# Kernel tuning notes

Hardware: AMD Instinct MI355X
Metric: run time of the kernel (lower is better)

The kernel has to match this reference:

```python
import jax, jax.numpy as jnp
import numpy as np

B, S, D, H, MLP = 8, 1024, 768, 12, 3072
HD = D // H
EPS = 1e-5


def setup_inputs() -> dict:
    key = jax.random.key(0)
    ks = jax.random.split(key, 5)
    sd = lambda fan_in: 1.0 / np.sqrt(fan_in)
    return {
        "x": jax.random.normal(ks[0], (B, S, D), jnp.float32),
        "w_qkv": jax.random.normal(ks[1], (D, 3 * D), jnp.float32) * sd(D),
        "w_out": jax.random.normal(ks[2], (D, D), jnp.float32) * sd(D),
        "b_out": jnp.zeros((D,), jnp.float32),
        "w1": jax.random.normal(ks[3], (D, MLP), jnp.float32) * sd(D),
        "b1": jnp.zeros((MLP,), jnp.float32),
        "w2": jax.random.normal(ks[4], (MLP, D), jnp.float32) * sd(MLP),
        "b2": jnp.zeros((D,), jnp.float32),
    }


def _instance_norm(x):
    # torch InstanceNorm2d on a 3D [B,S,D] tensor treats it as unbatched (C,H,W):
    # normalize over (S, D) per batch element, biased var, eps=1e-5, no affine.
    mu = jnp.mean(x, axis=(1, 2), keepdims=True)
    var = jnp.mean(jnp.square(x - mu), axis=(1, 2), keepdims=True)
    return (x - mu) * jax.lax.rsqrt(var + EPS)


def reference(x, w_qkv, w_out, b_out, w1, b1, w2, b2):
    scale = HD ** -0.5
    # --- self-attention branch ---
    h = _instance_norm(x)
    qkv = (h @ w_qkv).reshape(B, S, 3, H, HD)          # (qkv, heads, head_dim) split
    qkv = qkv.transpose(2, 0, 3, 1, 4)                  # [3, B, H, S, HD]
    q, k, v = qkv[0], qkv[1], qkv[2]
    att = jax.nn.softmax(jnp.einsum('bhxd,bhyd->bhxy', q, k) * scale, axis=-1)
    o = jnp.einsum('bhxy,bhyd->bhxd', att, v)           # [B, H, S, HD]
    o = o.transpose(0, 2, 1, 3).reshape(B, S, D)        # b h l d -> b l (h d)
    x = x + (o @ w_out + b_out)
    # --- MLP branch (exact erf GELU, as nn.GELU default) ---
    h2 = _instance_norm(x)
    m = jax.nn.gelu(h2 @ w1 + b1, approximate=False) @ w2 + b2
    return x + m
```

## Files before the change

kernel.cpp:

```cpp
#include <hip/hip_runtime.h>
#include <hip/hip_bf16.h>

typedef __hip_bfloat16 bf16;
typedef __attribute__((ext_vector_type(8))) short short8;
typedef __attribute__((ext_vector_type(4))) float f32x4;

#define B_   8
#define S_   1024
#define D_   768
#define H_   12
#define HD_  64
#define MLP_ 3072
#define SD_  (S_ * D_)

#define QSCALE 0.18033688011112042f

__device__ __forceinline__ float b2f(short h) {
  union { unsigned u; float f; } w;
  w.u = ((unsigned)(unsigned short)h) << 16;
  return w.f;
}

__device__ __forceinline__ float fast_exp2(float x) {
  float r;
  asm("v_exp_f32 %0, %1" : "=v"(r) : "v"(x));
  return r;
}

__device__ __forceinline__ bf16 fastbf(float f) {
  union { float f; unsigned u; } w; w.f = f;
  unsigned r = (w.u + 0x7FFF + ((w.u >> 16) & 1)) >> 16;
  union { unsigned short s; bf16 b; } o; o.s = (unsigned short)r;
  return o.b;
}

__device__ __forceinline__ void gl2lds16(const bf16* g, bf16* l) {
  __builtin_amdgcn_global_load_lds(
      (const __attribute__((address_space(1))) unsigned*)(const void*)g,
      (__attribute__((address_space(3))) unsigned*)(void*)l, 16, 0, 0);
}

__global__ __launch_bounds__(256) void transpose_all(
    const float* __restrict__ w_qkv, const float* __restrict__ w_out,
    const float* __restrict__ w1, const float* __restrict__ w2,
    bf16* __restrict__ t_qkv, bf16* __restrict__ t_out,
    bf16* __restrict__ t1, bf16* __restrict__ t2,
    float* __restrict__ zstats) {
  const int t = blockIdx.x;
  if (t == 0 && threadIdx.x < 32) zstats[threadIdx.x] = 0.f;
  const float* in; bf16* out; int R, C, idx;
  if (t < 1728)      { in = w_qkv; out = t_qkv; R = 768;  C = 2304; idx = t; }
  else if (t < 2304) { in = w_out; out = t_out; R = 768;  C = 768;  idx = t - 1728; }
  else if (t < 4608) { in = w1;    out = t1;    R = 768;  C = 3072; idx = t - 2304; }
  else               { in = w2;    out = t2;    R = 3072; C = 768;  idx = t - 4608; }
  const int nbx = C >> 5;
  const int bx = (idx % nbx) * 32, by = (idx / nbx) * 32;
  __shared__ float tt[32][33];
  const int tx = threadIdx.x & 31, ty = threadIdx.x >> 5;
#pragma unroll
  for (int rr = 0; rr < 32; rr += 8)
    tt[ty + rr][tx] = in[(long)(by + ty + rr) * C + bx + tx];
  __syncthreads();
#pragma unroll
  for (int rr = 0; rr < 32; rr += 8)
    out[(long)(bx + ty + rr) * R + by + tx] = __float2bfloat16(tt[tx][ty + rr]);
}

__global__ __launch_bounds__(256) void stats_partial(const float* __restrict__ x,
                                                     float* __restrict__ red_x,
                                                     const bf16* __restrict__ wt1,
                                                     const bf16* __restrict__ wt_qkv,
                                                     float* __restrict__ cs1,
                                                     float* __restrict__ csq,
                                                     bf16* __restrict__ xb) {
  if (blockIdx.x >= 768) {
    const bf16* wsrc; float* cdst; int bi;
    if (blockIdx.x < 816) { wsrc = wt1;    cdst = cs1; bi = blockIdx.x - 768; }
    else                  { wsrc = wt_qkv; cdst = csq; bi = blockIdx.x - 816; }
    const int row = bi * 64 + (threadIdx.x >> 2);
    const int part = threadIdx.x & 3;
    const bf16* wr = wsrc + (long)row * 768 + part * 192;
    float s = 0.f;
#pragma unroll
    for (int u = 0; u < 24; ++u) {
      short8 v = *(const short8*)(wr + u * 8);
#pragma unroll
      for (int e = 0; e < 8; ++e) s += b2f(v[e]);
    }
    s += __shfl_xor(s, 1, 64);
    s += __shfl_xor(s, 2, 64);
    if (part == 0) cdst[row] = s;
    return;
  }
  const long off = (long)blockIdx.x * 8192;
  float s = 0.f, s2 = 0.f;
#pragma unroll
  for (int it = 0; it < 4; ++it) {
    const long i = off + ((long)threadIdx.x + it * 256) * 8;
    float4 v0 = *(const float4*)(x + i);
    float4 v1 = *(const float4*)(x + i + 4);
    s += v0.x + v0.y + v0.z + v0.w + v1.x + v1.y + v1.z + v1.w;
    s2 += v0.x * v0.x + v0.y * v0.y + v0.z * v0.z + v0.w * v0.w +
          v1.x * v1.x + v1.y * v1.y + v1.z * v1.z + v1.w * v1.w;
    __align__(16) bf16 tmp[8];
    tmp[0] = __float2bfloat16(v0.x); tmp[1] = __float2bfloat16(v0.y);
    tmp[2] = __float2bfloat16(v0.z); tmp[3] = __float2bfloat16(v0.w);
    tmp[4] = __float2bfloat16(v1.x); tmp[5] = __float2bfloat16(v1.y);
    tmp[6] = __float2bfloat16(v1.z); tmp[7] = __float2bfloat16(v1.w);
    *(short8*)(xb + i) = *(const short8*)tmp;
  }
#pragma unroll
  for (int o = 1; o < 64; o <<= 1) { s += __shfl_xor(s, o, 64); s2 += __shfl_xor(s2, o, 64); }
  __shared__ float sh[8];
  const int wave = threadIdx.x >> 6, lane = threadIdx.x & 63;
  if (lane == 0) { sh[wave * 2] = s; sh[wave * 2 + 1] = s2; }
  __syncthreads();
  if (threadIdx.x == 0) {
    const int bb = blockIdx.x / 96;
    atomicAdd(&red_x[bb * 2],     sh[0] + sh[2] + sh[4] + sh[6]);
    atomicAdd(&red_x[bb * 2 + 1], sh[1] + sh[3] + sh[5] + sh[7]);
  }
}

template <int EPI, bool STATS>
__global__ __launch_bounds__(256) void gemm_k(
    const bf16* __restrict__ A, const bf16* __restrict__ Bt,
    int M, int N, int K,
    const float* __restrict__ biasf, const float* __restrict__ resf,
    const float* __restrict__ cs, const float* __restrict__ stat_in,
    float* __restrict__ outf,
    bf16* __restrict__ outb0, bf16* __restrict__ outb1, bf16* __restrict__ outb2,
    float* __restrict__ statp) {
  __shared__ __align__(16) bf16 As[128 * 64];
  __shared__ __align__(16) bf16 Bs[128 * 64];
  __shared__ float sred[8];
  const int tid = threadIdx.x;
  const int bm = blockIdx.x * 128, bn = blockIdx.y * 128;
  const int wave = tid >> 6, lane = tid & 63;
  const int quad = lane >> 4, l16 = lane & 15;
  const int wm = (wave >> 1) * 64, wn = (wave & 1) * 64;
  const int swz = l16 & 7;

  f32x4 acc[4][4];
#pragma unroll
  for (int i = 0; i < 4; ++i)
#pragma unroll
    for (int j = 0; j < 4; ++j) acc[i][j] = (f32x4){0.f, 0.f, 0.f, 0.f};

  const int srow = tid >> 3;
  const int sgc = (tid & 7) ^ (srow & 7);
  const bf16* Ab = A + (long)(bm + srow) * K + sgc * 8;
  const bf16* Bb = Bt + (long)(bn + srow) * K + sgc * 8;

  auto stage = [&](int k0) {
#pragma unroll
    for (int s = 0; s < 4; ++s)
      gl2lds16(Ab + (long)(s * 32) * K + k0, &As[0] + s * 2048 + tid * 8);
#pragma unroll
    for (int s = 0; s < 4; ++s)
      gl2lds16(Bb + (long)(s * 32) * K + k0, &Bs[0] + s * 2048 + tid * 8);
  };

  stage(0);
  const int nk = K >> 6;
  for (int kt = 0; kt < nk; ++kt) {
    __syncthreads();
    short8 a[2][4], b[2][4];
#pragma unroll
    for (int kk = 0; kk < 2; ++kk) {
      const int co = ((kk * 4 + quad) ^ swz) * 8;
#pragma unroll
      for (int i = 0; i < 4; ++i)
        a[kk][i] = *(const short8*)(&As[0] + (wm + i * 16 + l16) * 64 + co);
#pragma unroll
      for (int j = 0; j < 4; ++j)
        b[kk][j] = *(const short8*)(&Bs[0] + (wn + j * 16 + l16) * 64 + co);
    }
    __syncthreads();
    if (kt + 1 < nk) stage((kt + 1) * 64);
#pragma unroll
    for (int kk = 0; kk < 2; ++kk)
#pragma unroll
      for (int i = 0; i < 4; ++i)
#pragma unroll
        for (int j = 0; j < 4; ++j)
          acc[i][j] = __builtin_amdgcn_mfma_f32_16x16x32_bf16(a[kk][i], b[kk][j], acc[i][j], 0, 0, 0);
  }

  const int m0 = bm + wm + quad * 4;
  const int n0 = bn + wn + l16;
  const int batch = bm >> 10;
  float mu = 0.f, rs = 0.f;
  if (EPI == 0 || EPI == 2) {
    const float s1 = stat_in[batch * 2], s2v = stat_in[batch * 2 + 1];
    mu = s1 * (1.0f / SD_);
    rs = rsqrtf(s2v * (1.0f / SD_) - mu * mu + 1e-5f);
  }
  float ts = 0.f, ts2 = 0.f;
#pragma unroll
  for (int i = 0; i < 4; ++i) {
#pragma unroll
    for (int j = 0; j < 4; ++j) {
      const int n = n0 + j * 16;
#pragma unroll
      for (int r = 0; r < 4; ++r) {
        const int m = m0 + i * 16 + r;
        float v = acc[i][j][r];
        if (EPI == 0) {
          v = rs * (v - mu * cs[n]);
          const int t = n / D_;
          const int rr2 = n - t * D_;
          const int hh = rr2 >> 6, dd = rr2 & 63;
          const int bb = m >> 10, ss = m & 1023;
          const long hoff = (long)(bb * H_ + hh);
          if (t == 0)      outb0[(hoff * S_ + ss) * HD_ + dd] = __float2bfloat16(v * QSCALE);
          else if (t == 1) outb1[(hoff * S_ + ss) * HD_ + dd] = __float2bfloat16(v);
          else             outb2[(hoff * HD_ + dd) * S_ + ss] = __float2bfloat16(v);
        } else if (EPI == 1) {
          v += biasf[n] + resf[(long)m * N + n];
          outf[(long)m * N + n] = v;
          outb0[(long)m * N + n] = __float2bfloat16(v);
          if (STATS) { ts += v; ts2 += v * v; }
        } else if (EPI == 2) {
          v = rs * (v - mu * cs[n]) + biasf[n];
          float u = v * v;
          float y = v * (1.0f + 0.044715f * u) * 0.7978845608028654f;
          float z = fast_exp2(y * -2.885390081777927f);
          v = v * __builtin_amdgcn_rcpf(1.0f + z);
          outb0[(long)m * N + n] = __float2bfloat16(v);
        } else {
          v += biasf[n] + resf[(long)m * N + n];
          outf[(long)m * N + n] = v;
        }
      }
    }
  }
  if (STATS) {
#pragma unroll
    for (int o = 1; o < 64; o <<= 1) { ts += __shfl_xor(ts, o, 64); ts2 += __shfl_xor(ts2, o, 64); }
    if (lane == 0) { sred[wave * 2] = ts; sred[wave * 2 + 1] = ts2; }
    __syncthreads();
    if (tid == 0) {
      atomicAdd(&statp[batch * 2], sred[0] + sred[2] + sred[4] + sred[6]);
      atomicAdd(&statp[batch * 2 + 1], sred[1] + sred[3] + sred[5] + sred[7]);
    }
  }
}

__global__ __launch_bounds__(512) void attn64(const bf16* __restrict__ q,
                                              const bf16* __restrict__ k,
                                              const bf16* __restrict__ vt,
                                              bf16* __restrict__ o) {
  __shared__ __align__(16) bf16 Ks[2][64 * 64];
  __shared__ __align__(16) bf16 Vs[2][64 * 64];
  const int bh = blockIdx.x, qt = blockIdx.y;
  const int tid = threadIdx.x, wave = tid >> 6, lane = tid & 63;
  const int quad = lane >> 4, l16 = lane & 15;
  const int sw = (l16 & 7) ^ ((l16 >> 3) & 1);
  const long base = (long)bh * (S_ * HD_);
  const bf16* kg = k + base;
  const bf16* vg = vt + base;

  const int srow = tid >> 3;
  const int scg = (tid & 7) ^ (srow & 7) ^ ((srow >> 3) & 1);

  short8 aq[2];
#pragma unroll
  for (int kk = 0; kk < 2; ++kk)
    aq[kk] = *(const short8*)(q + base + (long)(qt * 128 + wave * 16 + l16) * HD_ +
                              kk * 32 + quad * 8);

  gl2lds16(kg + (long)srow * HD_ + scg * 8, &Ks[0][0] + tid * 8);
  gl2lds16(vg + (long)srow * S_ + scg * 8, &Vs[0][0] + tid * 8);

  const bf16* kp = kg + (long)(64 + srow) * HD_ + scg * 8;
  const bf16* vp = vg + (long)srow * S_ + 64 + scg * 8;

  f32x4 oacc[4];
#pragma unroll
  for (int j = 0; j < 4; ++j) oacc[j] = (f32x4){0.f, 0.f, 0.f, 0.f};
  float lp = 0.f;

  const int vh = (quad & 1) * 4;

#define ATTN_STEP(CUR, DOPREF)                                                 \
  {                                                                            \
    __syncthreads();                                                           \
    if (DOPREF) {               \
      gl2lds16(kp, &Ks[(CUR) ^ 1][0] + tid * 8);                               \
      gl2lds16(vp, &Vs[(CUR) ^ 1][0] + tid * 8);                               \
      kp += 64 * HD_;                                                          \
      vp += 64;                                                                \
    }                                                                          \
    f32x4 s[4];                                                                \
    _Pragma("unroll")                                                          \
    for (int i = 0; i < 4; ++i) s[i] = (f32x4){0.f, 0.f, 0.f, 0.f};            \
    _Pragma("unroll")                                                          \
    for (int kk = 0; kk < 2; ++kk) {                                           \
      _Pragma("unroll")                                                        \
      for (int i = 0; i < 4; ++i) {                                            \
        short8 ak = *(const short8*)(&Ks[CUR][0] + (i * 16 + l16) * 64 +       \
                                     (((kk * 4 + quad) ^ sw) * 8));            \
        s[i] = __builtin_amdgcn_mfma_f32_16x16x32_bf16(ak, aq[kk], s[i], 0, 0, 0); \
      }                                                                        \
    }                                                                          \
    float pe[4][4];                                                            \
    _Pragma("unroll")                                                          \
    for (int i = 0; i < 4; ++i) {                                              \
      _Pragma("unroll")                                                        \
      for (int r = 0; r < 4; ++r) { pe[i][r] = fast_exp2(s[i][r]); lp += pe[i][r]; } \
    }                                                                          \
    union { short8 v; bf16 b[8]; } af[2];                                      \
    _Pragma("unroll")                                                          \
    for (int r = 0; r < 4; ++r) {                                              \
      af[0].b[r]     = fastbf(pe[0][r]);                                       \
      af[0].b[4 + r] = fastbf(pe[1][r]);                                       \
      af[1].b[r]     = fastbf(pe[2][r]);                                       \
      af[1].b[4 + r] = fastbf(pe[3][r]);                                       \
    }                                                                          \
    _Pragma("unroll")                                                          \
    for (int kk = 0; kk < 2; ++kk) {                                           \
      const int g0 = ((4 * kk + (quad >> 1)) ^ sw) * 8 + vh;                   \
      const int g1 = ((4 * kk + 2 + (quad >> 1)) ^ sw) * 8 + vh;               \
      _Pragma("unroll")                                                        \
      for (int dj = 0; dj < 4; ++dj) {                                         \
        const bf16* vrow = &Vs[CUR][0] + (dj * 16 + l16) * 64;                 \
        union { short8 v; uint2 u[2]; } bv;                                    \
        bv.u[0] = *(const uint2*)(vrow + g0);                                  \
        bv.u[1] = *(const uint2*)(vrow + g1);                                  \
        oacc[dj] = __builtin_amdgcn_mfma_f32_16x16x32_bf16(af[kk].v, bv.v, oacc[dj], 0, 0, 0); \
      }                                                                        \
    }                                                                          \
  }

  for (int c = 0; c < 16; c += 2) {
    ATTN_STEP(0, true)
    ATTN_STEP(1, (c < 14))
  }
#undef ATTN_STEP

  float lt = lp;
  lt += __shfl_xor(lt, 16, 64);
  lt += __shfl_xor(lt, 32, 64);

  const int b = bh / H_, hh = bh - b * H_;
#pragma unroll
  for (int r = 0; r < 4; ++r) {
    const float inv = 1.0f / __shfl(lt, quad * 4 + r, 64);
    const int sg = qt * 128 + wave * 16 + quad * 4 + r;
    const long rowoff = ((long)b * S_ + sg) * D_ + hh * HD_;
#pragma unroll
    for (int dj = 0; dj < 4; ++dj)
      o[rowoff + dj * 16 + l16] = __float2bfloat16(oacc[dj][r] * inv);
  }
}

extern "C" void kernel_launch(void* const* d_in, const int* in_sizes, int n_in,
                              void* d_out, int out_size, void* d_ws, size_t ws_size,
                              hipStream_t stream) {
  const float* x     = (const float*)d_in[0];
  const float* w_qkv = (const float*)d_in[1];
  const float* w_out = (const float*)d_in[2];
  const float* b_out = (const float*)d_in[3];
  const float* w1    = (const float*)d_in[4];
  const float* b1    = (const float*)d_in[5];
  const float* w2    = (const float*)d_in[6];
  const float* b2    = (const float*)d_in[7];
  float* out = (float*)d_out;

  bf16* wt_qkv = (bf16*)d_ws;
  bf16* wt_out = wt_qkv + 2304 * 768;
  bf16* wt1    = wt_out + 768 * 768;
  bf16* wt2    = wt1 + 3072 * 768;
  bf16* qb     = wt2 + 768 * 3072;
  bf16* kb     = qb + 6291456;
  bf16* vtb    = kb + 6291456;
  bf16* ob     = vtb + 6291456;
  float* x1f   = (float*)(ob + 6291456);
  bf16* hb     = (bf16*)(x1f + 6291456);
  float* redp  = (float*)(hb + 6291456);
  float* red_x = redp + 1536;
  float* red2  = red_x + 16;
  float* cs1   = red2 + 16;
  float* csq   = cs1 + 3072;
  bf16* gb     = qb;
  bf16* xb     = hb;
  bf16* x1b    = hb;

  transpose_all<<<6912, 256, 0, stream>>>(w_qkv, w_out, w1, w2,
                                          wt_qkv, wt_out, wt1, wt2, red_x);

  stats_partial<<<768 + 48 + 36, 256, 0, stream>>>(x, red_x, wt1, wt_qkv,
                                                   cs1, csq, xb);

  gemm_k<0, false><<<dim3(64, 18), 256, 0, stream>>>(
      xb, wt_qkv, 8192, 2304, 768, nullptr, nullptr, csq, red_x,
      nullptr, qb, kb, vtb, nullptr);
  attn64<<<dim3(B_ * H_, 8), 512, 0, stream>>>(qb, kb, vtb, ob);

  gemm_k<1, true><<<dim3(64, 6), 256, 0, stream>>>(
      ob, wt_out, 8192, 768, 768, b_out, x, nullptr, nullptr,
      x1f, x1b, nullptr, nullptr, red2);

  gemm_k<2, false><<<dim3(64, 24), 256, 0, stream>>>(
      x1b, wt1, 8192, 3072, 768, b1, nullptr, cs1, red2,
      nullptr, gb, nullptr, nullptr, nullptr);

  gemm_k<3, false><<<dim3(64, 6), 256, 0, stream>>>(
      gb, wt2, 8192, 768, 3072, b2, x1f, nullptr, nullptr,
      out, nullptr, nullptr, nullptr, nullptr);
}
```

Baseline: 341.7 us.

## Merge weight transpose and input stats into one kernel; add attention MFMA priority hints

Fuses the weight transpose/convert kernel with the input-statistics and column-sum work into a single launch. Column sums are now computed directly from the fp32 weights with bf16 rounding, removing the dependency on the transposed output. Per-block partial sums replace atomics, and the QKV GEMM reduces the 96 partials per batch in its epilogue. The attention loop also wraps its MFMA sections in s_setprio hints. The trade-offs are strided, poorly coalesced column-sum loads in a few long-running blocks and a redundant 96-element reduction in every GEMM block.

Result: slower. 352.5 us (+3.2%).

```diff
diff --git a/kernel.cpp b/kernel.cpp
--- a/kernel.cpp
+++ b/kernel.cpp
@@ -34,20 +34,74 @@
   return o.b;
 }
 
+__device__ __forceinline__ float roundbf(float f) {
+  union { float f; unsigned u; } w; w.f = f;
+  w.u = ((w.u + 0x7FFF + ((w.u >> 16) & 1)) >> 16) << 16;
+  return w.f;
+}
+
 __device__ __forceinline__ void gl2lds16(const bf16* g, bf16* l) {
   __builtin_amdgcn_global_load_lds(
       (const __attribute__((address_space(1))) unsigned*)(const void*)g,
       (__attribute__((address_space(3))) unsigned*)(void*)l, 16, 0, 0);
 }
 
-__global__ __launch_bounds__(256) void transpose_all(
+__global__ __launch_bounds__(256) void transpose_stats(
     const float* __restrict__ w_qkv, const float* __restrict__ w_out,
     const float* __restrict__ w1, const float* __restrict__ w2,
     bf16* __restrict__ t_qkv, bf16* __restrict__ t_out,
     bf16* __restrict__ t1, bf16* __restrict__ t2,
-    float* __restrict__ zstats) {
+    const float* __restrict__ x, bf16* __restrict__ xb,
+    float* __restrict__ redp, float* __restrict__ cs1, float* __restrict__ csq,
+    float* __restrict__ red2) {
   const int t = blockIdx.x;
-  if (t == 0 && threadIdx.x < 32) zstats[threadIdx.x] = 0.f;
+  if (t == 0 && threadIdx.x < 16) red2[threadIdx.x] = 0.f;
+
+  if (t >= 7680) {
+    const float* wsrc; float* cdst; int C, n0;
+    if (t < 7692) { wsrc = w1;    cdst = cs1; C = 3072; n0 = (t - 7680) * 256; }
+    else          { wsrc = w_qkv; cdst = csq; C = 2304; n0 = (t - 7692) * 256; }
+    const int n = n0 + threadIdx.x;
+    float s = 0.f;
+#pragma unroll 8
+    for (int k = 0; k < 768; ++k)
+      s += roundbf(wsrc[(long)k * C + n]);
+    cdst[n] = s;
+    return;
+  }
+
+  if (t >= 6912) {
+    const int bi = t - 6912;
+    const long off = (long)bi * 8192;
+    float s = 0.f, s2 = 0.f;
+#pragma unroll
+    for (int it = 0; it < 4; ++it) {
+      const long i = off + ((long)threadIdx.x + it * 256) * 8;
+      float4 v0 = *(const float4*)(x + i);
+      float4 v1 = *(const float4*)(x + i + 4);
+      s += v0.x + v0.y + v0.z + v0.w + v1.x + v1.y + v1.z + v1.w;
+      s2 += v0.x * v0.x + v0.y * v0.y + v0.z * v0.z + v0.w * v0.w +
+            v1.x * v1.x + v1.y * v1.y + v1.z * v1.z + v1.w * v1.w;
+      __align__(16) bf16 tmp[8];
+      tmp[0] = __float2bfloat16(v0.x); tmp[1] = __float2bfloat16(v0.y);
+      tmp[2] = __float2bfloat16(v0.z); tmp[3] = __float2bfloat16(v0.w);
+      tmp[4] = __float2bfloat16(v1.x); tmp[5] = __float2bfloat16(v1.y);
+      tmp[6] = __float2bfloat16(v1.z); tmp[7] = __float2bfloat16(v1.w);
+      *(short8*)(xb + i) = *(const short8*)tmp;
+    }
+#pragma unroll
+    for (int o = 1; o < 64; o <<= 1) { s += __shfl_xor(s, o, 64); s2 += __shfl_xor(s2, o, 64); }
+    __shared__ float sh[8];
+    const int wave = threadIdx.x >> 6, lane = threadIdx.x & 63;
+    if (lane == 0) { sh[wave * 2] = s; sh[wave * 2 + 1] = s2; }
+    __syncthreads();
+    if (threadIdx.x == 0) {
+      redp[bi * 2]     = sh[0] + sh[2] + sh[4] + sh[6];
+      redp[bi * 2 + 1] = sh[1] + sh[3] + sh[5] + sh[7];
+    }
+    return;
+  }
+
   const float* in; bf16* out; int R, C, idx;
   if (t < 1728)      { in = w_qkv; out = t_qkv; R = 768;  C = 2304; idx = t; }
   else if (t < 2304) { in = w_out; out = t_out; R = 768;  C = 768;  idx = t - 1728; }
@@ -64,62 +118,6 @@
 #pragma unroll
   for (int rr = 0; rr < 32; rr += 8)
     out[(long)(bx + ty + rr) * R + by + tx] = __float2bfloat16(tt[tx][ty + rr]);
-}
-
-__global__ __launch_bounds__(256) void stats_partial(const float* __restrict__ x,
-                                                     float* __restrict__ red_x,
-                                                     const bf16* __restrict__ wt1,
-                                                     const bf16* __restrict__ wt_qkv,
-                                                     float* __restrict__ cs1,
-                                                     float* __restrict__ csq,
-                                                     bf16* __restrict__ xb) {
-  if (blockIdx.x >= 768) {
-    const bf16* wsrc; float* cdst; int bi;
-    if (blockIdx.x < 816) { wsrc = wt1;    cdst = cs1; bi = blockIdx.x - 768; }
-    else                  { wsrc = wt_qkv; cdst = csq; bi = blockIdx.x - 816; }
-    const int row = bi * 64 + (threadIdx.x >> 2);
-    const int part = threadIdx.x & 3;
-    const bf16* wr = wsrc + (long)row * 768 + part * 192;
-    float s = 0.f;
-#pragma unroll
-    for (int u = 0; u < 24; ++u) {
-      short8 v = *(const short8*)(wr + u * 8);
-#pragma unroll
-      for (int e = 0; e < 8; ++e) s += b2f(v[e]);
-    }
-    s += __shfl_xor(s, 1, 64);
-    s += __shfl_xor(s, 2, 64);
-    if (part == 0) cdst[row] = s;
-    return;
-  }
-  const long off = (long)blockIdx.x * 8192;
-  float s = 0.f, s2 = 0.f;
-#pragma unroll
-  for (int it = 0; it < 4; ++it) {
-    const long i = off + ((long)threadIdx.x + it * 256) * 8;
-    float4 v0 = *(const float4*)(x + i);
-    float4 v1 = *(const float4*)(x + i + 4);
-    s += v0.x + v0.y + v0.z + v0.w + v1.x + v1.y + v1.z + v1.w;
-    s2 += v0.x * v0.x + v0.y * v0.y + v0.z * v0.z + v0.w * v0.w +
-          v1.x * v1.x + v1.y * v1.y + v1.z * v1.z + v1.w * v1.w;
-    __align__(16) bf16 tmp[8];
-    tmp[0] = __float2bfloat16(v0.x); tmp[1] = __float2bfloat16(v0.y);
-    tmp[2] = __float2bfloat16(v0.z); tmp[3] = __float2bfloat16(v0.w);
-    tmp[4] = __float2bfloat16(v1.x); tmp[5] = __float2bfloat16(v1.y);
-    tmp[6] = __float2bfloat16(v1.z); tmp[7] = __float2bfloat16(v1.w);
-    *(short8*)(xb + i) = *(const short8*)tmp;
-  }
-#pragma unroll
-  for (int o = 1; o < 64; o <<= 1) { s += __shfl_xor(s, o, 64); s2 += __shfl_xor(s2, o, 64); }
-  __shared__ float sh[8];
-  const int wave = threadIdx.x >> 6, lane = threadIdx.x & 63;
-  if (lane == 0) { sh[wave * 2] = s; sh[wave * 2 + 1] = s2; }
-  __syncthreads();
-  if (threadIdx.x == 0) {
-    const int bb = blockIdx.x / 96;
-    atomicAdd(&red_x[bb * 2],     sh[0] + sh[2] + sh[4] + sh[6]);
-    atomicAdd(&red_x[bb * 2 + 1], sh[1] + sh[3] + sh[5] + sh[7]);
-  }
 }
 
 template <int EPI, bool STATS>
@@ -191,7 +189,14 @@
   const int n0 = bn + wn + l16;
   const int batch = bm >> 10;
   float mu = 0.f, rs = 0.f;
-  if (EPI == 0 || EPI == 2) {
+  if (EPI == 0) {
+    float s1 = 0.f, s2v = 0.f;
+    const float* pp = stat_in + batch * 192;
+#pragma unroll 8
+    for (int k = 0; k < 96; ++k) { s1 += pp[k * 2]; s2v += pp[k * 2 + 1]; }
+    mu = s1 * (1.0f / SD_);
+    rs = rsqrtf(s2v * (1.0f / SD_) - mu * mu + 1e-5f);
+  } else if (EPI == 2) {
     const float s1 = stat_in[batch * 2], s2v = stat_in[batch * 2 + 1];
     mu = s1 * (1.0f / SD_);
     rs = rsqrtf(s2v * (1.0f / SD_) - mu * mu + 1e-5f);
@@ -295,6 +300,7 @@
     f32x4 s[4];                                                                \
     _Pragma("unroll")                                                          \
     for (int i = 0; i < 4; ++i) s[i] = (f32x4){0.f, 0.f, 0.f, 0.f};            \
+    __builtin_amdgcn_s_setprio(1);                                             \
     _Pragma("unroll")                                                          \
     for (int kk = 0; kk < 2; ++kk) {                                           \
       _Pragma("unroll")                                                        \
@@ -304,6 +310,7 @@
         s[i] = __builtin_amdgcn_mfma_f32_16x16x32_bf16(ak, aq[kk], s[i], 0, 0, 0); \
       }                                                                        \
     }                                                                          \
+    __builtin_amdgcn_s_setprio(0);                                             \
     float pe[4][4];                                                            \
     _Pragma("unroll")                                                          \
     for (int i = 0; i < 4; ++i) {                                              \
@@ -318,6 +325,7 @@
       af[1].b[r]     = fastbf(pe[2][r]);                                       \
       af[1].b[4 + r] = fastbf(pe[3][r]);                                       \
     }                                                                          \
+    __builtin_amdgcn_s_setprio(1);                                             \
     _Pragma("unroll")                                                          \
     for (int kk = 0; kk < 2; ++kk) {                                           \
       const int g0 = ((4 * kk + (quad >> 1)) ^ sw) * 8 + vh;                   \
@@ -331,6 +339,7 @@
         oacc[dj] = __builtin_amdgcn_mfma_f32_16x16x32_bf16(af[kk].v, bv.v, oacc[dj], 0, 0, 0); \
       }                                                                        \
     }                                                                          \
+    __builtin_amdgcn_s_setprio(0);                                             \
   }
 
   for (int c = 0; c < 16; c += 2) {
@@ -387,14 +396,12 @@
   bf16* xb     = hb;
   bf16* x1b    = hb;
 
-  transpose_all<<<6912, 256, 0, stream>>>(w_qkv, w_out, w1, w2,
-                                          wt_qkv, wt_out, wt1, wt2, red_x);
-
-  stats_partial<<<768 + 48 + 36, 256, 0, stream>>>(x, red_x, wt1, wt_qkv,
-                                                   cs1, csq, xb);
+  transpose_stats<<<7701, 256, 0, stream>>>(w_qkv, w_out, w1, w2,
+                                            wt_qkv, wt_out, wt1, wt2,
+                                            x, xb, redp, cs1, csq, red2);
 
   gemm_k<0, false><<<dim3(64, 18), 256, 0, stream>>>(
-      xb, wt_qkv, 8192, 2304, 768, nullptr, nullptr, csq, red_x,
+      xb, wt_qkv, 8192, 2304, 768, nullptr, nullptr, csq, redp,
       nullptr, qb, kb, vtb, nullptr);
   attn64<<<dim3(B_ * H_, 8), 512, 0, stream>>>(qb, kb, vtb, ob);
 
```
